# Optimization experiments

Measured on AMD Instinct MI355X. Metric: run time of the kernel, lower is better.

The kernel has to match this reference:

```python
import jax, jax.numpy as jnp
import numpy as np

B, T, C, H, D = 2, 2048, 768, 12, 64
ATTN_MULT = 0.125  # 1/sqrt(head_dim)


def setup_inputs() -> dict:
    key = jax.random.key(0)
    k0, k1, k2 = jax.random.split(key, 3)
    x = jax.random.normal(k0, (B, T, C), jnp.float32)
    w_attn = jax.random.normal(k1, (3 * H * D, C), jnp.float32) * 0.02
    b_attn = jnp.zeros((3 * H * D,), jnp.float32)
    w_proj = jax.random.normal(k2, (C, H * D), jnp.float32) * 0.02
    b_proj = jnp.zeros((C,), jnp.float32)
    return {"x": x, "w_attn": w_attn, "b_attn": b_attn, "w_proj": w_proj, "b_proj": b_proj}


def reference(x, w_attn, b_attn, w_proj, b_proj):
    Bx, Tx, Cx = x.shape
    # fused qkv projection (torch nn.Linear: x @ W^T + b)
    qkv = x @ w_attn.T + b_attn                      # [B,T,3*H*D]
    q, k, v = jnp.split(qkv, 3, axis=2)
    def to_heads(t):
        return t.reshape(Bx, Tx, H, D).transpose(0, 2, 1, 3)  # [B,H,T,D]
    q, k, v = to_heads(q), to_heads(k), to_heads(v)
    att = jnp.einsum('bhqd,bhkd->bhqk', q, k) * ATTN_MULT     # [B,H,T,T]

    causal = jnp.tril(jnp.ones((Tx, Tx), dtype=bool))
    # selection scores from head 0 (selective attention)
    S = jax.nn.relu(att[:, 0])                                # [B,T,T]
    # prevent_from_masking_myself: zero diagonal; protect_bos_token: zero key col 0
    smask = causal & ~jnp.eye(Tx, dtype=bool)
    smask = smask.at[:, 0].set(False)
    S = jnp.where(smask, S, 0.0)
    # exclusive cumulative sum over the query dim: F[i,j] = sum_{i'<i} S[i',j]
    Fmask = jnp.cumsum(S, axis=-2) - S                        # [B,T,T]
    att = att - Fmask[:, None]                                # broadcast over heads

    att = jnp.where(causal, att, -jnp.inf)
    p = jax.nn.softmax(att, axis=-1)                          # [B,H,T,T]
    y = jnp.einsum('bhqk,bhkd->bhqd', p, v)                   # [B,H,T,D]
    y = y.transpose(0, 2, 1, 3).reshape(Bx, Tx, H * D)
    return y @ w_proj.T + b_proj
```

## Files before the change

kernel.cpp:

```cpp
#include <hip/hip_runtime.h>
#include <hip/hip_bf16.h>

#define BB 2
#define TT 2048
#define CC 768
#define HH 12
#define DD 64
#define NQKV 2304
#define MTOT (BB*TT)
#define CH 32
#define NCH (TT/CH)

typedef __bf16 bf16x8 __attribute__((ext_vector_type(8)));
typedef __bf16 bf16x4 __attribute__((ext_vector_type(4)));
typedef float  f32x4  __attribute__((ext_vector_type(4)));

__device__ __forceinline__ f32x4 mfma16(bf16x8 a, bf16x8 b, f32x4 c) {
    return __builtin_amdgcn_mfma_f32_16x16x32_bf16(a, b, c, 0, 0, 0);
}

__device__ __forceinline__ void load_lds16(const void* g, void* l) {
    __builtin_amdgcn_global_load_lds(
        (const __attribute__((address_space(1))) void*)g,
        (__attribute__((address_space(3))) void*)l, 16, 0, 0);
}

__global__ __launch_bounds__(256) void cvt_bf16_kernel(
    const float* __restrict__ x, const float* __restrict__ wa, const float* __restrict__ wp,
    __bf16* __restrict__ xb, __bf16* __restrict__ wab, __bf16* __restrict__ wpb)
{
    const long NX = (long)MTOT * CC;
    const long NWA = (long)NQKV * CC;
    long idx = ((long)blockIdx.x * 256 + threadIdx.x) * 4;
    const float* src; __bf16* dst; long off;
    if (idx < NX)            { src = x;  dst = xb;  off = idx; }
    else if (idx < NX + NWA) { src = wa; dst = wab; off = idx - NX; }
    else                     { src = wp; dst = wpb; off = idx - NX - NWA; }
    float4 v = *(const float4*)(src + off);
    bf16x4 o;
    o[0] = (__bf16)v.x; o[1] = (__bf16)v.y; o[2] = (__bf16)v.z; o[3] = (__bf16)v.w;
    *(bf16x4*)(dst + off) = o;
}

template<int EPI>
__global__ __launch_bounds__(256, 2) void gemm_nt_kernel(
    const __bf16* __restrict__ A, const __bf16* __restrict__ Bw,
    const float* __restrict__ bias,
    __bf16* __restrict__ oQ, __bf16* __restrict__ oK, __bf16* __restrict__ oVT,
    float* __restrict__ oOut, int K)
{
    __shared__ __align__(16) __bf16 As[128 * 32];
    __shared__ __align__(16) __bf16 Bs[128 * 32];
    const int tid = threadIdx.x;
    const int m0 = blockIdx.y * 128, n0 = blockIdx.x * 128;
    const int w = tid >> 6, lane = tid & 63, quad = lane >> 4, l16 = lane & 15;
    const int wm = (w >> 1) * 64, wn = (w & 1) * 64;
    const int grow = w * 16 + (lane >> 2);
    const int gcol = (lane & 3) * 8;
    __bf16* AsW = As + w * 512;
    __bf16* BsW = Bs + w * 512;

    f32x4 acc[4][4] = {};

    for (int kt = 0; kt < K; kt += 32) {
        __syncthreads();
        load_lds16(A  + (long)(m0 + grow) * K + kt + gcol,      AsW);
        load_lds16(A  + (long)(m0 + grow + 64) * K + kt + gcol, AsW + 2048);
        load_lds16(Bw + (long)(n0 + grow) * K + kt + gcol,      BsW);
        load_lds16(Bw + (long)(n0 + grow + 64) * K + kt + gcol, BsW + 2048);
        __syncthreads();

        bf16x8 af[4], bfr[4];
#pragma unroll
        for (int g = 0; g < 4; g++)  af[g]  = *(const bf16x8*)(As + (wm + g * 16 + l16) * 32 + quad * 8);
#pragma unroll
        for (int jb = 0; jb < 4; jb++) bfr[jb] = *(const bf16x8*)(Bs + (wn + jb * 16 + l16) * 32 + quad * 8);
#pragma unroll
        for (int g = 0; g < 4; g++)
#pragma unroll
            for (int jb = 0; jb < 4; jb++)
                acc[g][jb] = mfma16(af[g], bfr[jb], acc[g][jb]);
    }

#pragma unroll
    for (int jb = 0; jb < 4; jb++) {
        const int n = n0 + wn + jb * 16 + l16;
        const float bv = bias[n];
#pragma unroll
        for (int g = 0; g < 4; g++) {
#pragma unroll
            for (int r = 0; r < 4; r++) {
                const int m = m0 + wm + g * 16 + quad * 4 + r;
                const float v = acc[g][jb][r] + bv;
                if (EPI == 0) {
                    const int which = n / 768;
                    const int rem = n - which * 768;
                    const int h = rem >> 6, d = rem & 63;
                    const int b = m >> 11, t = m & 2047;
                    const __bf16 hv = (__bf16)v;
                    if (which == 0)      oQ [(((b * HH + h) * TT + t) << 6) + d] = hv;
                    else if (which == 1) oK [(((b * HH + h) * TT + t) << 6) + d] = hv;
                    else                 oVT[((((b * HH + h) << 6) + d) * TT) + t] = hv;
                } else {
                    oOut[(long)m * CC + n] = v;
                }
            }
        }
    }
}

__global__ __launch_bounds__(256) void sgemm_kernel(
    const __bf16* __restrict__ q, const __bf16* __restrict__ k, __bf16* __restrict__ S)
{
    const int tj = blockIdx.x, ti = blockIdx.y, b = blockIdx.z;
    if (tj > ti) return;
    const int w = threadIdx.x >> 6, lane = threadIdx.x & 63, quad = lane >> 4, l16 = lane & 15;
    const int i0 = ti * 64 + w * 16;

    const __bf16* qp = q + (((long)(b * HH + 0) * TT + i0 + l16) << 6) + quad * 8;
    bf16x8 a0 = *(const bf16x8*)qp, a1 = *(const bf16x8*)(qp + 32);
    const __bf16* kbase = k + ((long)(b * HH + 0) * TT << 6);

#pragma unroll
    for (int jb = 0; jb < 4; jb++) {
        const __bf16* kp = kbase + (((long)(tj * 64 + jb * 16 + l16)) << 6) + quad * 8;
        bf16x8 b0 = *(const bf16x8*)kp, b1 = *(const bf16x8*)(kp + 32);
        f32x4 acc = {};
        acc = mfma16(a0, b0, acc);
        acc = mfma16(a1, b1, acc);
        const int j = tj * 64 + jb * 16 + l16;
#pragma unroll
        for (int r = 0; r < 4; r++) {
            const int i = i0 + quad * 4 + r;
            float v = fmaxf(acc[r] * 0.125f, 0.0f);
            v = (j >= 1 && j < i) ? v : 0.0f;
            S[((long)b * TT + i) * TT + j] = (__bf16)v;
        }
    }
}

__global__ __launch_bounds__(256) void scan_sum_kernel(
    const __bf16* __restrict__ S, float* __restrict__ csum)
{
    const int j = blockIdx.x * 256 + threadIdx.x;
    const int chunk = blockIdx.y, b = blockIdx.z;
    const int ib = chunk * CH;
    const __bf16* p = S + ((long)b * TT + ib) * TT + j;
    float s = 0.0f;
#pragma unroll
    for (int ii = 0; ii < CH; ii++) {
        float v = (float)p[(long)ii * TT];
        s += ((ib + ii) > j) ? v : 0.0f;
    }
    csum[(b * NCH + chunk) * TT + j] = s;
}

__global__ __launch_bounds__(256) void scan_prefix_kernel(float* __restrict__ csum)
{
    const int idx = blockIdx.x * 256 + threadIdx.x;
    const int b = idx >> 11, j = idx & 2047;
    float vals[NCH];
#pragma unroll
    for (int c = 0; c < NCH; c++) vals[c] = csum[(b * NCH + c) * TT + j];
    float off = 0.0f;
#pragma unroll
    for (int c = 0; c < NCH; c++) { float t = vals[c]; vals[c] = off; off += t; }
#pragma unroll
    for (int c = 0; c < NCH; c++) csum[(b * NCH + c) * TT + j] = vals[c];
}

__global__ __launch_bounds__(256) void scan_write_kernel(
    const __bf16* __restrict__ S, const float* __restrict__ csum, __bf16* __restrict__ Fo)
{
    const int j = blockIdx.x * 256 + threadIdx.x;
    const int chunk = blockIdx.y, b = blockIdx.z;
    const int ib = chunk * CH;
    float off = csum[(b * NCH + chunk) * TT + j];
    const __bf16* ps = S  + ((long)b * TT + ib) * TT + j;
    __bf16*       pf = Fo + ((long)b * TT + ib) * TT + j;
#pragma unroll
    for (int ii = 0; ii < CH; ii++) {
        float v = ((ib + ii) > j) ? (float)ps[(long)ii * TT] : 0.0f;
        pf[(long)ii * TT] = (__bf16)off;
        off += v;
    }
}

__global__ __launch_bounds__(128, 2) void flash_kernel(
    const __bf16* __restrict__ q, const __bf16* __restrict__ k, const __bf16* __restrict__ vT,
    const __bf16* __restrict__ F, __bf16* __restrict__ y)
{
    __shared__ __align__(16) __bf16 Ks[64 * 64];
    __shared__ __align__(16) __bf16 Vs[64 * 64];
    __shared__ __align__(16) __bf16 Pls[2][16 * 72];
    const int bid = blockIdx.x, h = blockIdx.y, b = blockIdx.z;
    const int w = threadIdx.x >> 6, lane = threadIdx.x & 63, quad = lane >> 4, l16 = lane & 15;
    const int rl = lane >> 3;
    const int cs8 = ((lane & 7) ^ rl) * 8;
    __bf16* KsW = Ks + w * 2048;
    __bf16* VsW = Vs + w * 2048;
    const int sw0 = ((quad)     ^ (l16 & 7)) * 8;
    const int sw1 = ((quad + 4) ^ (l16 & 7)) * 8;
    __bf16* Pl = &Pls[w][0];
    const __bf16* kb = k  + ((long)(b * HH + h) * TT << 6);
    const __bf16* vb = vT + ((long)(b * HH + h) * TT << 6);

    for (int ph = 0; ph < 2; ph++) {
        const int qt = ph ? (63 - bid) : bid;
        const int i0 = qt * 32 + w * 16;
        const __bf16* qp = q + (((long)(b * HH + h) * TT + i0 + l16) << 6) + quad * 8;
        const bf16x8 aq0 = *(const bf16x8*)qp;
        const bf16x8 aq1 = *(const bf16x8*)(qp + 32);
        const __bf16* Fb = F + (long)b * TT * TT + (long)i0 * TT;
        f32x4 O[4] = {};
        float lr[4] = {0.0f, 0.0f, 0.0f, 0.0f};
        const int jtend = (qt >> 1) << 6;

        for (int jt = 0; jt <= jtend; jt += 64) {
            __syncthreads();
#pragma unroll
            for (int t = 0; t < 4; t++)
                load_lds16(kb + ((long)(jt + w * 32 + t * 8 + rl) << 6) + cs8, KsW + t * 512);
#pragma unroll
            for (int t = 0; t < 4; t++)
                load_lds16(vb + (long)(w * 32 + t * 8 + rl) * TT + jt + cs8, VsW + t * 512);
            float Fc[4][4];
#pragma unroll
            for (int jh = 0; jh < 4; jh++)
#pragma unroll
                for (int r = 0; r < 4; r++)
                    Fc[jh][r] = (float)Fb[(long)(quad * 4 + r) * TT + jt + jh * 16 + l16];
            __syncthreads();
            float sc[4][4];
#pragma unroll
            for (int jh = 0; jh < 4; jh++) {
                const int jr = jh * 16 + l16;
                const bf16x8 kc0 = *(const bf16x8*)(Ks + (jr << 6) + sw0);
                const bf16x8 kc1 = *(const bf16x8*)(Ks + (jr << 6) + sw1);
                f32x4 acc = {};
                acc = mfma16(aq0, kc0, acc);
                acc = mfma16(aq1, kc1, acc);
#pragma unroll
                for (int r = 0; r < 4; r++) sc[jh][r] = acc[r];
            }
            if (jt == jtend) {
#pragma unroll
                for (int jh = 0; jh < 4; jh++) {
                    const int j = jt + jh * 16 + l16;
#pragma unroll
                    for (int r = 0; r < 4; r++) {
                        const int i = i0 + quad * 4 + r;
                        float v = fmaf(sc[jh][r], 0.125f, -Fc[jh][r]);
                        v = (j <= i) ? v : -1e30f;
                        const float p = __expf(fminf(v, 60.0f));
                        sc[jh][r] = p;
                        lr[r] += p;
                    }
                }
            } else {
#pragma unroll
                for (int jh = 0; jh < 4; jh++) {
#pragma unroll
                    for (int r = 0; r < 4; r++) {
                        float v = fmaf(sc[jh][r], 0.125f, -Fc[jh][r]);
                        const float p = __expf(fminf(v, 60.0f));
                        sc[jh][r] = p;
                        lr[r] += p;
                    }
                }
            }
#pragma unroll
            for (int r = 0; r < 4; r++) {
                const int il = quad * 4 + r;
#pragma unroll
                for (int jh = 0; jh < 4; jh++)
                    Pl[il * 72 + jh * 16 + l16] = (__bf16)sc[jh][r];
            }
            const bf16x8 ap0 = *(const bf16x8*)(Pl + l16 * 72 + quad * 8);
            const bf16x8 ap1 = *(const bf16x8*)(Pl + l16 * 72 + 32 + quad * 8);
#pragma unroll
            for (int db = 0; db < 4; db++) {
                const bf16x8 vv0 = *(const bf16x8*)(Vs + ((db * 16 + l16) << 6) + sw0);
                const bf16x8 vv1 = *(const bf16x8*)(Vs + ((db * 16 + l16) << 6) + sw1);
                O[db] = mfma16(ap0, vv0, O[db]);
                O[db] = mfma16(ap1, vv1, O[db]);
            }
        }

        float inv[4];
#pragma unroll
        for (int r = 0; r < 4; r++) {
            float s = lr[r];
#pragma unroll
            for (int off = 8; off >= 1; off >>= 1) s += __shfl_xor(s, off, 16);
            inv[r] = 1.0f / s;
        }
#pragma unroll
        for (int db = 0; db < 4; db++) {
#pragma unroll
            for (int r = 0; r < 4; r++) {
                const int i = i0 + quad * 4 + r;
                y[((long)(b * TT + i)) * (HH * DD) + h * 64 + db * 16 + l16] = (__bf16)(O[db][r] * inv[r]);
            }
        }
    }
}

extern "C" void kernel_launch(void* const* d_in, const int* in_sizes, int n_in,
                              void* d_out, int out_size, void* d_ws, size_t ws_size,
                              hipStream_t stream)
{
    const float* x      = (const float*)d_in[0];
    const float* w_attn = (const float*)d_in[1];
    const float* b_attn = (const float*)d_in[2];
    const float* w_proj = (const float*)d_in[3];
    const float* b_proj = (const float*)d_in[4];
    float* out = (float*)d_out;

    char* ws = (char*)d_ws;
    __bf16* xb  = (__bf16*)ws; ws += (long)MTOT * CC * 2;
    __bf16* wab = (__bf16*)ws; ws += (long)NQKV * CC * 2;
    __bf16* wpb = (__bf16*)ws; ws += (long)CC * (HH*DD) * 2;
    __bf16* qb  = (__bf16*)ws; ws += (long)BB * HH * TT * DD * 2;
    __bf16* kb  = (__bf16*)ws; ws += (long)BB * HH * TT * DD * 2;
    __bf16* vtb = (__bf16*)ws; ws += (long)BB * HH * TT * DD * 2;
    __bf16* SF  = (__bf16*)ws; ws += (long)BB * TT * TT * 2;
    __bf16* Fo  = (__bf16*)ws; ws += (long)BB * TT * TT * 2;
    float*  cs  = (float*)ws;  ws += (long)BB * NCH * TT * 4;
    __bf16* yb  = (__bf16*)ws; ws += (long)MTOT * (HH*DD) * 2;

    cvt_bf16_kernel<<<5376, 256, 0, stream>>>(x, w_attn, w_proj, xb, wab, wpb);
    gemm_nt_kernel<0><<<dim3(NQKV / 128, MTOT / 128), 256, 0, stream>>>(
        xb, wab, b_attn, qb, kb, vtb, nullptr, CC);
    sgemm_kernel<<<dim3(TT / 64, TT / 64, BB), 256, 0, stream>>>(qb, kb, SF);
    scan_sum_kernel<<<dim3(TT / 256, NCH, BB), 256, 0, stream>>>(SF, cs);
    scan_prefix_kernel<<<16, 256, 0, stream>>>(cs);
    scan_write_kernel<<<dim3(TT / 256, NCH, BB), 256, 0, stream>>>(SF, cs, Fo);
    flash_kernel<<<dim3(32, HH, BB), 128, 0, stream>>>(qb, kb, vtb, Fo, yb);
    gemm_nt_kernel<1><<<dim3((HH*DD) / 128, MTOT / 128), 256, 0, stream>>>(
        yb, wpb, b_proj, nullptr, nullptr, nullptr, out, HH * DD);
}
```

Measured before the change: 220.1 us.

## Double-buffer K/V tiles and prefetch F across a flattened two-phase loop

Flattens the two query-tile phases of the flash kernel into one loop and double-buffers the K and V shared-memory tiles. The next tile's K/V and F values are fetched before computing on the current tile, and one of the two barriers per iteration is dropped. It also removes the exp clamp and uses a finite mask value. The cost is twice the shared memory, which may reduce occupancy, plus more register pressure from the prefetched F values.

```diff
diff --git a/kernel.cpp b/kernel.cpp
--- a/kernel.cpp
+++ b/kernel.cpp
@@ -190,117 +190,167 @@
     const __bf16* __restrict__ q, const __bf16* __restrict__ k, const __bf16* __restrict__ vT,
     const __bf16* __restrict__ F, __bf16* __restrict__ y)
 {
-    __shared__ __align__(16) __bf16 Ks[64 * 64];
-    __shared__ __align__(16) __bf16 Vs[64 * 64];
+    __shared__ __align__(16) __bf16 Ks[2][64 * 64];
+    __shared__ __align__(16) __bf16 Vs[2][64 * 64];
     __shared__ __align__(16) __bf16 Pls[2][16 * 72];
     const int bid = blockIdx.x, h = blockIdx.y, b = blockIdx.z;
     const int w = threadIdx.x >> 6, lane = threadIdx.x & 63, quad = lane >> 4, l16 = lane & 15;
     const int rl = lane >> 3;
     const int cs8 = ((lane & 7) ^ rl) * 8;
-    __bf16* KsW = Ks + w * 2048;
-    __bf16* VsW = Vs + w * 2048;
     const int sw0 = ((quad)     ^ (l16 & 7)) * 8;
     const int sw1 = ((quad + 4) ^ (l16 & 7)) * 8;
     __bf16* Pl = &Pls[w][0];
     const __bf16* kb = k  + ((long)(b * HH + h) * TT << 6);
     const __bf16* vb = vT + ((long)(b * HH + h) * TT << 6);
-
-    for (int ph = 0; ph < 2; ph++) {
-        const int qt = ph ? (63 - bid) : bid;
-        const int i0 = qt * 32 + w * 16;
-        const __bf16* qp = q + (((long)(b * HH + h) * TT + i0 + l16) << 6) + quad * 8;
-        const bf16x8 aq0 = *(const bf16x8*)qp;
-        const bf16x8 aq1 = *(const bf16x8*)(qp + 32);
-        const __bf16* Fb = F + (long)b * TT * TT + (long)i0 * TT;
-        f32x4 O[4] = {};
-        float lr[4] = {0.0f, 0.0f, 0.0f, 0.0f};
+    const __bf16* Fbase = F + (long)b * TT * TT;
+
+    const int qt0 = bid, qt1 = 63 - bid;
+    const int n0 = (qt0 >> 1) + 1, n1 = (qt1 >> 1) + 1;
+    const int N = n0 + n1;
+
+    int i0 = qt0 * 32 + w * 16;
+    const __bf16* qp = q + (((long)(b * HH + h) * TT + i0 + l16) << 6) + quad * 8;
+    bf16x8 aq0 = *(const bf16x8*)qp;
+    bf16x8 aq1 = *(const bf16x8*)(qp + 32);
+
+    f32x4 O[4] = {};
+    float lr[4] = {0.0f, 0.0f, 0.0f, 0.0f};
+    __bf16 Fn[4][4];
+
+    {
+        __bf16* KsW = Ks[0] + w * 2048;
+        __bf16* VsW = Vs[0] + w * 2048;
+#pragma unroll
+        for (int t = 0; t < 4; t++)
+            load_lds16(kb + ((long)(w * 32 + t * 8 + rl) << 6) + cs8, KsW + t * 512);
+#pragma unroll
+        for (int t = 0; t < 4; t++)
+            load_lds16(vb + (long)(w * 32 + t * 8 + rl) * TT + cs8, VsW + t * 512);
+        const __bf16* Fb = Fbase + (long)i0 * TT;
+#pragma unroll
+        for (int jh = 0; jh < 4; jh++)
+#pragma unroll
+            for (int r = 0; r < 4; r++)
+                Fn[jh][r] = Fb[(long)(quad * 4 + r) * TT + jh * 16 + l16];
+    }
+
+    for (int it = 0; it < N; it++) {
+        const int ph = (it >= n0);
+        const int jt = (it - (ph ? n0 : 0)) << 6;
+        const int qt = ph ? qt1 : qt0;
         const int jtend = (qt >> 1) << 6;
 
-        for (int jt = 0; jt <= jtend; jt += 64) {
-            __syncthreads();
+        __syncthreads();
+
+        __bf16 Fc[4][4];
+#pragma unroll
+        for (int jh = 0; jh < 4; jh++)
+#pragma unroll
+            for (int r = 0; r < 4; r++)
+                Fc[jh][r] = Fn[jh][r];
+
+        if (it + 1 < N) {
+            const int ph2 = (it + 1 >= n0);
+            const int jt2 = ((it + 1) - (ph2 ? n0 : 0)) << 6;
+            __bf16* KsW = Ks[(it + 1) & 1] + w * 2048;
+            __bf16* VsW = Vs[(it + 1) & 1] + w * 2048;
 #pragma unroll
             for (int t = 0; t < 4; t++)
-                load_lds16(kb + ((long)(jt + w * 32 + t * 8 + rl) << 6) + cs8, KsW + t * 512);
+                load_lds16(kb + ((long)(jt2 + w * 32 + t * 8 + rl) << 6) + cs8, KsW + t * 512);
 #pragma unroll
             for (int t = 0; t < 4; t++)
-                load_lds16(vb + (long)(w * 32 + t * 8 + rl) * TT + jt + cs8, VsW + t * 512);
-            float Fc[4][4];
+                load_lds16(vb + (long)(w * 32 + t * 8 + rl) * TT + jt2 + cs8, VsW + t * 512);
+            const int i0n = (ph2 ? qt1 : qt0) * 32 + w * 16;
+            const __bf16* Fb2 = Fbase + (long)i0n * TT;
 #pragma unroll
             for (int jh = 0; jh < 4; jh++)
 #pragma unroll
                 for (int r = 0; r < 4; r++)
-                    Fc[jh][r] = (float)Fb[(long)(quad * 4 + r) * TT + jt + jh * 16 + l16];
-            __syncthreads();
-            float sc[4][4];
+                    Fn[jh][r] = Fb2[(long)(quad * 4 + r) * TT + jt2 + jh * 16 + l16];
+        }
+        __builtin_amdgcn_sched_barrier(0);
+
+        const __bf16* Kc = Ks[it & 1];
+        const __bf16* Vc = Vs[it & 1];
+        float sc[4][4];
+#pragma unroll
+        for (int jh = 0; jh < 4; jh++) {
+            const int jr = jh * 16 + l16;
+            const bf16x8 kc0 = *(const bf16x8*)(Kc + (jr << 6) + sw0);
+            const bf16x8 kc1 = *(const bf16x8*)(Kc + (jr << 6) + sw1);
+            f32x4 acc = {};
+            acc = mfma16(aq0, kc0, acc);
+            acc = mfma16(aq1, kc1, acc);
+#pragma unroll
+            for (int r = 0; r < 4; r++) sc[jh][r] = acc[r];
+        }
+        if (jt == jtend) {
 #pragma unroll
             for (int jh = 0; jh < 4; jh++) {
-                const int jr = jh * 16 + l16;
-                const bf16x8 kc0 = *(const bf16x8*)(Ks + (jr << 6) + sw0);
-                const bf16x8 kc1 = *(const bf16x8*)(Ks + (jr << 6) + sw1);
-                f32x4 acc = {};
-                acc = mfma16(aq0, kc0, acc);
-                acc = mfma16(aq1, kc1, acc);
-#pragma unroll
-                for (int r = 0; r < 4; r++) sc[jh][r] = acc[r];
-            }
-            if (jt == jtend) {
-#pragma unroll
-                for (int jh = 0; jh < 4; jh++) {
-                    const int j = jt + jh * 16 + l16;
-#pragma unroll
-                    for (int r = 0; r < 4; r++) {
-                        const int i = i0 + quad * 4 + r;
-                        float v = fmaf(sc[jh][r], 0.125f, -Fc[jh][r]);
-                        v = (j <= i) ? v : -1e30f;
-                        const float p = __expf(fminf(v, 60.0f));
-                        sc[jh][r] = p;
-                        lr[r] += p;
-                    }
+                const int j = jt + jh * 16 + l16;
+#pragma unroll
+                for (int r = 0; r < 4; r++) {
+                    const int i = i0 + quad * 4 + r;
+                    float v = fmaf(sc[jh][r], 0.125f, -(float)Fc[jh][r]);
+                    v = (j <= i) ? v : -35.0f;
+                    const float p = __expf(v);
+                    sc[jh][r] = p;
+                    lr[r] += p;
                 }
-            } else {
-#pragma unroll
-                for (int jh = 0; jh < 4; jh++) {
-#pragma unroll
-                    for (int r = 0; r < 4; r++) {
-                        float v = fmaf(sc[jh][r], 0.125f, -Fc[jh][r]);
-                        const float p = __expf(fminf(v, 60.0f));
-                        sc[jh][r] = p;
-                        lr[r] += p;
-                    }
+            }
+        } else {
+#pragma unroll
+            for (int jh = 0; jh < 4; jh++) {
+#pragma unroll
+                for (int r = 0; r < 4; r++) {
+                    float v = fmaf(sc[jh][r], 0.125f, -(float)Fc[jh][r]);
+                    const float p = __expf(v);
+                    sc[jh][r] = p;
+                    lr[r] += p;
                 }
             }
+        }
+#pragma unroll
+        for (int r = 0; r < 4; r++) {
+            const int il = quad * 4 + r;
+#pragma unroll
+            for (int jh = 0; jh < 4; jh++)
+                Pl[il * 72 + jh * 16 + l16] = (__bf16)sc[jh][r];
+        }
+        const bf16x8 ap0 = *(const bf16x8*)(Pl + l16 * 72 + quad * 8);
+        const bf16x8 ap1 = *(const bf16x8*)(Pl + l16 * 72 + 32 + quad * 8);
+#pragma unroll
+        for (int db = 0; db < 4; db++) {
+            const bf16x8 vv0 = *(const bf16x8*)(Vc + ((db * 16 + l16) << 6) + sw0);
+            const bf16x8 vv1 = *(const bf16x8*)(Vc + ((db * 16 + l16) << 6) + sw1);
+            O[db] = mfma16(ap0, vv0, O[db]);
+            O[db] = mfma16(ap1, vv1, O[db]);
+        }
+        if (jt == jtend) {
+            float inv[4];
 #pragma unroll
             for (int r = 0; r < 4; r++) {
-                const int il = quad * 4 + r;
-#pragma unroll
-                for (int jh = 0; jh < 4; jh++)
-                    Pl[il * 72 + jh * 16 + l16] = (__bf16)sc[jh][r];
-            }
-            const bf16x8 ap0 = *(const bf16x8*)(Pl + l16 * 72 + quad * 8);
-            const bf16x8 ap1 = *(const bf16x8*)(Pl + l16 * 72 + 32 + quad * 8);
+                float s = lr[r];
+#pragma unroll
+                for (int off = 8; off >= 1; off >>= 1) s += __shfl_xor(s, off, 16);
+                inv[r] = 1.0f / s;
+            }
 #pragma unroll
             for (int db = 0; db < 4; db++) {
-                const bf16x8 vv0 = *(const bf16x8*)(Vs + ((db * 16 + l16) << 6) + sw0);
-                const bf16x8 vv1 = *(const bf16x8*)(Vs + ((db * 16 + l16) << 6) + sw1);
-                O[db] = mfma16(ap0, vv0, O[db]);
-                O[db] = mfma16(ap1, vv1, O[db]);
-            }
-        }
-
-        float inv[4];
-#pragma unroll
-        for (int r = 0; r < 4; r++) {
-            float s = lr[r];
-#pragma unroll
-            for (int off = 8; off >= 1; off >>= 1) s += __shfl_xor(s, off, 16);
-            inv[r] = 1.0f / s;
-        }
-#pragma unroll
-        for (int db = 0; db < 4; db++) {
-#pragma unroll
-            for (int r = 0; r < 4; r++) {
-                const int i = i0 + quad * 4 + r;
-                y[((long)(b * TT + i)) * (HH * DD) + h * 64 + db * 16 + l16] = (__bf16)(O[db][r] * inv[r]);
+#pragma unroll
+                for (int r = 0; r < 4; r++) {
+                    const int i = i0 + quad * 4 + r;
+                    y[((long)(b * TT + i)) * (HH * DD) + h * 64 + db * 16 + l16] = (__bf16)(O[db][r] * inv[r]);
+                }
+            }
+#pragma unroll
+            for (int db = 0; db < 4; db++) { O[db][0] = 0.f; O[db][1] = 0.f; O[db][2] = 0.f; O[db][3] = 0.f; }
+            lr[0] = lr[1] = lr[2] = lr[3] = 0.0f;
+            if (!ph) {
+                i0 = qt1 * 32 + w * 16;
+                const __bf16* qp2 = q + (((long)(b * HH + h) * TT + i0 + l16) << 6) + quad * 8;
+                aq0 = *(const bf16x8*)qp2;
+                aq1 = *(const bf16x8*)(qp2 + 32);
             }
         }
     }
```

Measured after the change: 224.9 us. 2.2% more time.
